# Kernel optimization log

Hardware: AMD Instinct MI355X
Metric: run time of the kernel (lower is better)

The kernel has to match this reference:

```python
import jax, jax.numpy as jnp
import numpy as np


def setup_inputs() -> dict:
    key = jax.random.key(0)
    ks = jax.random.split(key, 9)
    B, D, E, H, C = 8192, 1024, 8, 4096, 10
    s = lambda fan_in: 1.0 / np.sqrt(fan_in)
    return {
        "x":  jax.random.normal(ks[0], (B, D), jnp.float32),
        "Wr": jax.random.normal(ks[1], (D, E), jnp.float32) * s(D),
        "br": jnp.zeros((E,), jnp.float32),
        "W1": jax.random.normal(ks[2], (E, D, H), jnp.float32) * s(D),
        "b1": jnp.zeros((E, H), jnp.float32),
        "W2": jax.random.normal(ks[3], (E, H, D), jnp.float32) * s(H),
        "b2": jnp.zeros((E, D), jnp.float32),
        "Wc": jax.random.normal(ks[4], (D, C), jnp.float32) * s(D),
        "bc": jnp.zeros((C,), jnp.float32),
    }


def reference(x, Wr, br, W1, b1, W2, b2, Wc, bc):
    # Dense (no-topology) MoE path: softmax routing over all experts.
    routing = jax.nn.softmax(x @ Wr + br, axis=-1)          # [B, E]
    # All experts run on every token (dense all-expert loop, vectorized).
    h = jax.nn.relu(jnp.einsum('bd,edh->ebh', x, W1) + b1[:, None, :])  # [E, B, H]
    y = jnp.einsum('ebh,ehd->ebd', h, W2) + b2[:, None, :]              # [E, B, D]
    # Routing-weighted accumulation: sum_e y[e] * routing[:, e]
    out = jnp.einsum('ebd,be->bd', y, routing)              # [B, D]
    return out @ Wc + bc                                    # [B, C]
```

## Files before the change

### kernel.cpp

```cpp
#include <hip/hip_runtime.h>
#include <cstdint>
#include <cstddef>

using bf16x8 = __attribute__((ext_vector_type(8))) short;
using f32x4  = __attribute__((ext_vector_type(4))) float;

constexpr int kB = 8192;
constexpr int kD = 1024;
constexpr int kE = 8;
constexpr int kH = 4096;
constexpr int kC = 10;

__device__ __forceinline__ unsigned short f2bf(float f) {
  unsigned int u = __float_as_uint(f);
  u += 0x7FFFu + ((u >> 16) & 1u);
  return (unsigned short)(u >> 16);
}

#define GLD16(gptr, lptr)                                                      \
  __builtin_amdgcn_global_load_lds(                                            \
      (const __attribute__((address_space(1))) void*)(gptr),                   \
      (__attribute__((address_space(3))) void*)(lptr), 16, 0, 0)

__global__ __launch_bounds__(256) void k_convert_x(const float* __restrict__ x,
                                                   unsigned short* __restrict__ xb) {
  const long i = ((long)blockIdx.x * 256 + threadIdx.x) * 8;
  float4 a = *reinterpret_cast<const float4*>(x + i);
  float4 b = *reinterpret_cast<const float4*>(x + i + 4);
  bf16x8 o;
  o[0] = (short)f2bf(a.x); o[1] = (short)f2bf(a.y);
  o[2] = (short)f2bf(a.z); o[3] = (short)f2bf(a.w);
  o[4] = (short)f2bf(b.x); o[5] = (short)f2bf(b.y);
  o[6] = (short)f2bf(b.z); o[7] = (short)f2bf(b.w);
  *reinterpret_cast<bf16x8*>(xb + i) = o;
}

__global__ __launch_bounds__(256) void k_transpose_w(const float* __restrict__ W,
                                                     unsigned short* __restrict__ Wt,
                                                     int K, int N) {
  __shared__ unsigned short tile[32][33];
  const int e = blockIdx.z;
  const int n0 = blockIdx.x * 32, k0 = blockIdx.y * 32;
  const int tx = threadIdx.x, ty = threadIdx.y;
  const float* Wb = W + (size_t)e * K * N;
  unsigned short* Wtb = Wt + (size_t)e * N * K;
#pragma unroll
  for (int j = 0; j < 32; j += 8)
    tile[ty + j][tx] = f2bf(Wb[(size_t)(k0 + ty + j) * N + n0 + tx]);
  __syncthreads();
#pragma unroll
  for (int j = 0; j < 32; j += 8)
    Wtb[(size_t)(n0 + ty + j) * K + k0 + tx] = tile[tx][ty + j];
}

__global__ __launch_bounds__(256) void k_routing(const float* __restrict__ x,
                                                 const float* __restrict__ Wr,
                                                 const float* __restrict__ br,
                                                 float* __restrict__ r) {
  const int w = threadIdx.x >> 6, l = threadIdx.x & 63;
  const int b = blockIdx.x * 4 + w;
  const float* xr = x + (size_t)b * kD;
  float acc[kE];
#pragma unroll
  for (int e = 0; e < kE; ++e) acc[e] = 0.f;
  for (int d = l; d < kD; d += 64) {
    const float xv = xr[d];
    const float* wrow = Wr + d * kE;
#pragma unroll
    for (int e = 0; e < kE; ++e) acc[e] += xv * wrow[e];
  }
#pragma unroll
  for (int e = 0; e < kE; ++e) {
#pragma unroll
    for (int s = 32; s > 0; s >>= 1) acc[e] += __shfl_xor(acc[e], s);
    acc[e] += br[e];
  }
  float mx = acc[0];
#pragma unroll
  for (int e = 1; e < kE; ++e) mx = fmaxf(mx, acc[e]);
  float sum = 0.f;
#pragma unroll
  for (int e = 0; e < kE; ++e) { acc[e] = expf(acc[e] - mx); sum += acc[e]; }
  const float inv = 1.f / sum;
  float val = 0.f;
#pragma unroll
  for (int e = 0; e < kE; ++e) if (l == e) val = acc[e] * inv;
  if (l < kE) r[(size_t)b * kE + l] = val;
}

__global__ __launch_bounds__(128) void k_vbuild(const float* __restrict__ W2,
                                                const float* __restrict__ Wc,
                                                unsigned short* __restrict__ Vt) {
  __shared__ float WcL[kD * kC];
  for (int i = threadIdx.x; i < kD * kC; i += 128) WcL[i] = Wc[i];
  __syncthreads();
  const int gid = blockIdx.x * 128 + threadIdx.x;
  const int e = gid >> 12, hrow = gid & 4095;
  const float4* w2row = reinterpret_cast<const float4*>(W2 + (size_t)gid * kD);
  float acc[kC];
#pragma unroll
  for (int c = 0; c < kC; ++c) acc[c] = 0.f;
  for (int i = 0; i < kD / 4; ++i) {
    float4 w = w2row[i];
    const float* wc0 = WcL + (i * 4) * kC;
#pragma unroll
    for (int c = 0; c < kC; ++c)
      acc[c] += w.x * wc0[c] + w.y * wc0[kC + c] + w.z * wc0[2 * kC + c] +
                w.w * wc0[3 * kC + c];
  }
  unsigned short* vte = Vt + (size_t)e * 16 * kH;
#pragma unroll
  for (int c = 0; c < kC; ++c) vte[(size_t)c * kH + hrow] = f2bf(acc[c]);
#pragma unroll
  for (int c = kC; c < 16; ++c) vte[(size_t)c * kH + hrow] = 0;
}

__global__ __launch_bounds__(128) void k_ubuild(const float* __restrict__ b2,
                                                const float* __restrict__ Wc,
                                                float* __restrict__ u) {
  const int t = threadIdx.x;
  if (t >= kE * kC) return;
  const int e = t / kC, c = t % kC;
  float acc = 0.f;
  for (int d = 0; d < kD; ++d) acc += b2[e * kD + d] * Wc[d * kC + c];
  u[e * 16 + c] = acc;
}

__global__ __launch_bounds__(256) void k_zero_f32(float* __restrict__ p) {
  p[(size_t)blockIdx.x * 256 + threadIdx.x] = 0.f;
}

__global__ __launch_bounds__(512, 2) void k_moe_fused256(
    const unsigned short* __restrict__ xb,
    const unsigned short* __restrict__ W1t,
    const float* __restrict__ b1,
    const unsigned short* __restrict__ Vt,
    const float* __restrict__ rr,
    float* __restrict__ part) {
  __shared__ __align__(16) char smem[131072];
  constexpr int K = kD;
  constexpr int NIT = K / 128;

  const int e = blockIdx.z;
  const int bx = (blockIdx.x & 7) * 4 + (blockIdx.x >> 3);
  const int brow = bx * 256, bcol = blockIdx.y * 256;
  const unsigned short* const At = xb;
  const unsigned short* const Bt = W1t + (size_t)e * kH * kD;

  const int tid = threadIdx.x;
  const int w = tid >> 6, l = tid & 63;
  const int wr = w >> 2, wc = w & 3;
  const int fr = l & 15, jg = l >> 4;

  int ck[2];
#pragma unroll
  for (int k = 0; k < 2; ++k) ck[k] = (((k * 4 + jg) ^ (fr & 7)) << 4);
  const int abase = wr * 16384;
  const int bbase = 32768 + (wc >> 1) * 16384;
  const int brow0 = (wc & 1) * 64;

  const int p0 = w * 64 + l;
  const int rp = p0 >> 3;
  const int cs = (p0 & 7) ^ (rp & 7);
  const size_t aofs = (size_t)(brow + rp) * K + cs * 8;
  const size_t bofs = (size_t)(bcol + rp) * K + cs * 8;
  const int ldst = w * 1024;

#define STG_A(buf, ht, kt)                                                     \
  do {                                                                         \
    GLD16(At + aofs + (size_t)(ht) * 131072 + (size_t)(kt) * 64,               \
          smem + (buf) * 65536 + (ht) * 16384 + ldst);                         \
    GLD16(At + aofs + (size_t)(ht) * 131072 + 65536 + (size_t)(kt) * 64,       \
          smem + (buf) * 65536 + (ht) * 16384 + 8192 + ldst);                  \
  } while (0)
#define STG_B(buf, ht, kt)                                                     \
  do {                                                                         \
    GLD16(Bt + bofs + (size_t)(ht) * 131072 + (size_t)(kt) * 64,               \
          smem + (buf) * 65536 + 32768 + (ht) * 16384 + ldst);                 \
    GLD16(Bt + bofs + (size_t)(ht) * 131072 + 65536 + (size_t)(kt) * 64,       \
          smem + (buf) * 65536 + 32768 + (ht) * 16384 + 8192 + ldst);          \
  } while (0)

#define READ_A(buf, mp)                                                        \
  do {                                                                         \
    _Pragma("unroll") for (int mm = 0; mm < 2; ++mm)                           \
    _Pragma("unroll") for (int k = 0; k < 2; ++k)                              \
      aq[mm][k] = *reinterpret_cast<const bf16x8*>(                            \
          smem + (buf) * 65536 + abase + (((mp) * 2 + mm) * 16 + fr) * 128 + ck[k]); \
  } while (0)
#define READ_B(buf)                                                            \
  do {                                                                         \
    _Pragma("unroll") for (int n = 0; n < 4; ++n)                              \
    _Pragma("unroll") for (int k = 0; k < 2; ++k)                              \
      bq[n][k] = *reinterpret_cast<const bf16x8*>(                             \
          smem + (buf) * 65536 + bbase + (brow0 + n * 16 + fr) * 128 + ck[k]); \
  } while (0)
#define MFMA16(mp)                                                             \
  do {                                                                         \
    __builtin_amdgcn_s_setprio(1);                                             \
    _Pragma("unroll") for (int mm = 0; mm < 2; ++mm)                           \
    _Pragma("unroll") for (int n = 0; n < 4; ++n)                              \
    _Pragma("unroll") for (int k = 0; k < 2; ++k)                              \
      acc[(mp) * 2 + mm][n] = __builtin_amdgcn_mfma_f32_16x16x32_bf16(         \
          aq[mm][k], bq[n][k], acc[(mp) * 2 + mm][n], 0, 0, 0);                \
    __builtin_amdgcn_s_setprio(0);                                             \
  } while (0)
#define BARW() asm volatile("s_barrier\ns_waitcnt lgkmcnt(0)" ::: "memory")
#define BARP() asm volatile("s_barrier" ::: "memory")

  bf16x8 aq[2][2], bq[4][2];
  f32x4 acc[8][4];
#pragma unroll
  for (int m = 0; m < 8; ++m)
#pragma unroll
    for (int n = 0; n < 4; ++n) acc[m][n] = (f32x4){0.f, 0.f, 0.f, 0.f};

  STG_A(0, 0, 0); STG_A(0, 1, 0); STG_B(0, 0, 0); STG_B(0, 1, 0);
  STG_B(1, 0, 1); STG_B(1, 1, 1);
  asm volatile("s_waitcnt vmcnt(4)" ::: "memory");
  BARP();

  for (int i = 0; i < NIT; ++i) {
    const bool g = (i < NIT - 1);
    const int kx = 2 * i + 2, ky = 2 * i + 3;
    READ_A(0, 0); READ_B(0);
    STG_A(1, 0, 2 * i + 1);
    BARW(); MFMA16(0); BARP();
    READ_A(0, 1);
    STG_A(1, 1, 2 * i + 1);
    if (g) STG_B(0, 0, kx);
    BARW(); MFMA16(1); BARP();
    READ_A(0, 2);
    if (g) STG_B(0, 1, kx);
    BARW(); MFMA16(2); BARP();
    READ_A(0, 3);
    BARW(); MFMA16(3);
    if (g) asm volatile("s_waitcnt vmcnt(4)" ::: "memory");
    else   asm volatile("s_waitcnt vmcnt(0)" ::: "memory");
    BARP();
    READ_A(1, 0); READ_B(1);
    if (g) { STG_A(0, 0, kx); STG_A(0, 1, kx); }
    BARW(); MFMA16(0); BARP();
    READ_A(1, 1);
    if (g) STG_B(1, 0, ky);
    BARW(); MFMA16(1); BARP();
    READ_A(1, 2);
    if (g) STG_B(1, 1, ky);
    BARW(); MFMA16(2); BARP();
    READ_A(1, 3);
    BARW(); MFMA16(3);
    if (g) asm volatile("s_waitcnt vmcnt(4)" ::: "memory");
    BARP();
  }
#undef STG_A
#undef STG_B
#undef READ_A
#undef READ_B

#pragma unroll
  for (int n = 0; n < 4; ++n) {
    const int lcol = wc * 64 + n * 16 + fr;
    const float bias = b1[(size_t)e * kH + bcol + lcol];
    const int cbyte = (lcol >> 3) << 4;
#pragma unroll
    for (int m = 0; m < 8; ++m) {
#pragma unroll
      for (int j = 0; j < 4; ++j) {
        const int lrow = wr * 128 + m * 16 + jg * 4 + j;
        const float v = fmaxf(acc[m][n][j] + bias, 0.f);
        *reinterpret_cast<unsigned short*>(
            smem + lrow * 512 + (cbyte ^ ((lrow & 7) << 4)) + (fr & 7) * 2) = f2bf(v);
      }
    }
  }
  asm volatile("s_waitcnt lgkmcnt(0)\ns_barrier" ::: "memory");

  const unsigned short* const VtE = Vt + (size_t)e * 16 * kH + (size_t)fr * kH + bcol;
  bf16x8 gv[8];
#pragma unroll
  for (int kk = 0; kk < 8; ++kk)
    gv[kk] = *reinterpret_cast<const bf16x8*>(VtE + kk * 32 + jg * 8);
#pragma unroll
  for (int f = 0; f < 2; ++f) {
    const int rowl = (2 * w + f) * 16 + fr;
    f32x4 pc = (f32x4){0.f, 0.f, 0.f, 0.f};
#pragma unroll
    for (int kk = 0; kk < 8; ++kk) {
      bf16x8 ga = *reinterpret_cast<const bf16x8*>(
          smem + rowl * 512 + ((((kk * 4 + jg)) ^ (rowl & 7)) << 4));
      pc = __builtin_amdgcn_mfma_f32_16x16x32_bf16(ga, gv[kk], pc, 0, 0, 0);
    }
    const int rowg = brow + (2 * w + f) * 16 + jg * 4;
#pragma unroll
    for (int j = 0; j < 4; ++j) {
      const float val = pc[j] * rr[(size_t)(rowg + j) * kE + e];
      atomicAdd(&part[(size_t)(rowg + j) * 16 + fr], val);
    }
  }
}

__global__ __launch_bounds__(256) void k_combine(const float* __restrict__ part,
                                                 const float* __restrict__ rr,
                                                 const float* __restrict__ u,
                                                 const float* __restrict__ bc,
                                                 float* __restrict__ y) {
  const int tid = threadIdx.x;
  const int rloc = tid >> 4, c = tid & 15;
  const int b = blockIdx.x * 16 + rloc;
  if (c >= kC) return;
  float acc = part[(size_t)b * 16 + c] + bc[c];
#pragma unroll
  for (int e = 0; e < kE; ++e) acc += rr[(size_t)b * kE + e] * u[e * 16 + c];
  y[(size_t)b * kC + c] = acc;
}

extern "C" void kernel_launch(void* const* d_in, const int* in_sizes, int n_in,
                              void* d_out, int out_size, void* d_ws, size_t ws_size,
                              hipStream_t stream) {
  (void)in_sizes; (void)n_in; (void)out_size; (void)ws_size;
  const float* x  = (const float*)d_in[0];
  const float* Wr = (const float*)d_in[1];
  const float* br = (const float*)d_in[2];
  const float* W1 = (const float*)d_in[3];
  const float* b1 = (const float*)d_in[4];
  const float* W2 = (const float*)d_in[5];
  const float* b2 = (const float*)d_in[6];
  const float* Wc = (const float*)d_in[7];
  const float* bc = (const float*)d_in[8];
  float* y = (float*)d_out;

  char* p = (char*)d_ws;
  unsigned short* xb  = (unsigned short*)p; p += (size_t)kB * kD * 2;
  unsigned short* W1t = (unsigned short*)p; p += (size_t)kE * kH * kD * 2;
  unsigned short* Vt  = (unsigned short*)p; p += (size_t)kE * 16 * kH * 2;
  float* r    = (float*)p;                  p += (size_t)kB * kE * 4;
  float* u    = (float*)p;                  p += (size_t)kE * 16 * 4;
  float* part = (float*)p;                  p += (size_t)kB * 16 * 4;

  k_convert_x<<<dim3(kB * kD / 8 / 256), dim3(256), 0, stream>>>(x, xb);
  k_routing<<<dim3(kB / 4), dim3(256), 0, stream>>>(x, Wr, br, r);
  k_transpose_w<<<dim3(kH / 32, kD / 32, kE), dim3(32, 8), 0, stream>>>(W1, W1t, kD, kH);
  k_vbuild<<<dim3(kE * kH / 128), dim3(128), 0, stream>>>(W2, Wc, Vt);
  k_ubuild<<<dim3(1), dim3(128), 0, stream>>>(b2, Wc, u);
  k_zero_f32<<<dim3(kB * 16 / 256), dim3(256), 0, stream>>>(part);

  k_moe_fused256<<<dim3(kB / 256, kH / 256, kE), dim3(512), 0, stream>>>(
      xb, W1t, b1, Vt, r, part);

  k_combine<<<dim3(kB / 16), dim3(256), 0, stream>>>(part, r, u, bc, y);
}
```

Baseline: 697.8 us.

## Double-buffer LDS fragment registers to overlap ds_reads with MFMA in GEMM loop

The main expert GEMM loop now keeps two register sets for the A fragments and two for the B fragments. The LDS reads for the next sub-tile are issued before the MFMAs on the current one, with partial lgkmcnt waits and sched_barriers. Before, each phase read its fragments and then waited on lgkmcnt(0) right before the MFMAs. The aim is to hide LDS read latency behind matrix work. In exchange, register pressure rises and the hand-counted waitcnt values must match the number of outstanding LDS reads exactly, or the loop reads stale data.

Result: slower. 719.8 us (+3.2%).

```diff
diff --git a/kernel.cpp b/kernel.cpp
--- a/kernel.cpp
+++ b/kernel.cpp
@@ -181,34 +181,36 @@
           smem + (buf) * 65536 + 32768 + (ht) * 16384 + 8192 + ldst);          \
   } while (0)
 
-#define READ_A(buf, mp)                                                        \
+#define PREF_A(buf, mp, SET)                                                   \
   do {                                                                         \
     _Pragma("unroll") for (int mm = 0; mm < 2; ++mm)                           \
     _Pragma("unroll") for (int k = 0; k < 2; ++k)                              \
-      aq[mm][k] = *reinterpret_cast<const bf16x8*>(                            \
+      SET[mm][k] = *reinterpret_cast<const bf16x8*>(                           \
           smem + (buf) * 65536 + abase + (((mp) * 2 + mm) * 16 + fr) * 128 + ck[k]); \
   } while (0)
-#define READ_B(buf)                                                            \
+#define PREF_B(buf, SET)                                                       \
   do {                                                                         \
     _Pragma("unroll") for (int n = 0; n < 4; ++n)                              \
     _Pragma("unroll") for (int k = 0; k < 2; ++k)                              \
-      bq[n][k] = *reinterpret_cast<const bf16x8*>(                             \
+      SET[n][k] = *reinterpret_cast<const bf16x8*>(                            \
           smem + (buf) * 65536 + bbase + (brow0 + n * 16 + fr) * 128 + ck[k]); \
   } while (0)
-#define MFMA16(mp)                                                             \
+#define MFMA16(AQ, BQ, mp)                                                     \
   do {                                                                         \
     __builtin_amdgcn_s_setprio(1);                                             \
     _Pragma("unroll") for (int mm = 0; mm < 2; ++mm)                           \
     _Pragma("unroll") for (int n = 0; n < 4; ++n)                              \
     _Pragma("unroll") for (int k = 0; k < 2; ++k)                              \
       acc[(mp) * 2 + mm][n] = __builtin_amdgcn_mfma_f32_16x16x32_bf16(         \
-          aq[mm][k], bq[n][k], acc[(mp) * 2 + mm][n], 0, 0, 0);                \
+          AQ[mm][k], BQ[n][k], acc[(mp) * 2 + mm][n], 0, 0, 0);                \
     __builtin_amdgcn_s_setprio(0);                                             \
   } while (0)
-#define BARW() asm volatile("s_barrier\ns_waitcnt lgkmcnt(0)" ::: "memory")
-#define BARP() asm volatile("s_barrier" ::: "memory")
-
-  bf16x8 aq[2][2], bq[4][2];
+#define BAR()    asm volatile("s_barrier" ::: "memory")
+#define SCB()    __builtin_amdgcn_sched_barrier(0)
+#define WAITL(n) do { asm volatile("s_waitcnt lgkmcnt(" #n ")" ::: "memory"); SCB(); } while (0)
+#define WAITV(n) asm volatile("s_waitcnt vmcnt(" #n ")" ::: "memory")
+
+  bf16x8 aq0[2][2], aq1[2][2], bqX[4][2], bqY[4][2];
   f32x4 acc[8][4];
 #pragma unroll
   for (int m = 0; m < 8; ++m)
@@ -217,45 +219,72 @@
 
   STG_A(0, 0, 0); STG_A(0, 1, 0); STG_B(0, 0, 0); STG_B(0, 1, 0);
   STG_B(1, 0, 1); STG_B(1, 1, 1);
-  asm volatile("s_waitcnt vmcnt(4)" ::: "memory");
-  BARP();
+  WAITV(4);
+  BAR();
+  PREF_A(0, 0, aq0); PREF_B(0, bqX);
+  SCB();
 
   for (int i = 0; i < NIT; ++i) {
     const bool g = (i < NIT - 1);
     const int kx = 2 * i + 2, ky = 2 * i + 3;
-    READ_A(0, 0); READ_B(0);
     STG_A(1, 0, 2 * i + 1);
-    BARW(); MFMA16(0); BARP();
-    READ_A(0, 1);
+    BAR();
+    PREF_A(0, 1, aq1); SCB();
+    WAITL(4);
+    MFMA16(aq0, bqX, 0);
+    BAR();
     STG_A(1, 1, 2 * i + 1);
     if (g) STG_B(0, 0, kx);
-    BARW(); MFMA16(1); BARP();
-    READ_A(0, 2);
+    BAR();
+    PREF_A(0, 2, aq0); SCB();
+    WAITL(4);
+    MFMA16(aq1, bqX, 1);
+    BAR();
     if (g) STG_B(0, 1, kx);
-    BARW(); MFMA16(2); BARP();
-    READ_A(0, 3);
-    BARW(); MFMA16(3);
-    if (g) asm volatile("s_waitcnt vmcnt(4)" ::: "memory");
-    else   asm volatile("s_waitcnt vmcnt(0)" ::: "memory");
-    BARP();
-    READ_A(1, 0); READ_B(1);
+    BAR();
+    PREF_A(0, 3, aq1); SCB();
+    WAITL(4);
+    MFMA16(aq0, bqX, 2);
+    BAR();
+    if (g) WAITV(4); else WAITV(0);
+    BAR();
+    PREF_A(1, 0, aq0); PREF_B(1, bqY); SCB();
+    WAITL(12);
+    MFMA16(aq1, bqX, 3);
+    BAR();
     if (g) { STG_A(0, 0, kx); STG_A(0, 1, kx); }
-    BARW(); MFMA16(0); BARP();
-    READ_A(1, 1);
+    BAR();
+    PREF_A(1, 1, aq1); SCB();
+    WAITL(4);
+    MFMA16(aq0, bqY, 0);
+    BAR();
     if (g) STG_B(1, 0, ky);
-    BARW(); MFMA16(1); BARP();
-    READ_A(1, 2);
+    BAR();
+    PREF_A(1, 2, aq0); SCB();
+    WAITL(4);
+    MFMA16(aq1, bqY, 1);
+    BAR();
     if (g) STG_B(1, 1, ky);
-    BARW(); MFMA16(2); BARP();
-    READ_A(1, 3);
-    BARW(); MFMA16(3);
-    if (g) asm volatile("s_waitcnt vmcnt(4)" ::: "memory");
-    BARP();
+    BAR();
+    PREF_A(1, 3, aq1); SCB();
+    WAITL(4);
+    MFMA16(aq0, bqY, 2);
+    BAR();
+    if (g) WAITV(4);
+    BAR();
+    if (g) {
+      PREF_A(0, 0, aq0); PREF_B(0, bqX); SCB();
+      WAITL(12);
+    } else {
+      WAITL(0);
+    }
+    MFMA16(aq1, bqY, 3);
+    BAR();
   }
 #undef STG_A
 #undef STG_B
-#undef READ_A
-#undef READ_B
+#undef PREF_A
+#undef PREF_B
 
 #pragma unroll
   for (int n = 0; n < 4; ++n) {
@@ -297,6 +326,11 @@
       atomicAdd(&part[(size_t)(rowg + j) * 16 + fr], val);
     }
   }
+#undef MFMA16
+#undef BAR
+#undef SCB
+#undef WAITL
+#undef WAITV
 }
 
 __global__ __launch_bounds__(256) void k_combine(const float* __restrict__ part,
```
